# Performance work log

Hardware: AMD Instinct MI355X
Metric: run time of the kernel (lower is better)

The kernel has to match this reference:

```python
import jax, jax.numpy as jnp
import numpy as np

# dims: batch, length, n_values, input_dim, hidden_dim, embed_dim
B, L, V, D_IN, H, E = 8192, 32, 256, 256, 512, 256


def setup_inputs() -> dict:
    key = jax.random.key(0)
    ks = jax.random.split(key, 11)
    s = 0.05  # keep gates/tanh in a reasonable range
    return {
        "x": jax.random.normal(ks[0], (B, D_IN), jnp.float32),
        "emb": jax.random.normal(ks[1], (V, E), jnp.float32) * s,      # nn.Embedding weight
        "sos_embed": jax.random.normal(ks[2], (E,), jnp.float32) * s,
        "W_i2h": jax.random.normal(ks[3], (H, D_IN), jnp.float32) * s,  # input2hidden[0]
        "b_i2h": jax.random.normal(ks[4], (H,), jnp.float32) * s,
        "W_ih": jax.random.normal(ks[5], (3 * H, E), jnp.float32) * s,  # GRU weight_ih_l0 (r,z,n)
        "W_hh": jax.random.normal(ks[6], (3 * H, H), jnp.float32) * s,  # GRU weight_hh_l0
        "b_ih": jax.random.normal(ks[7], (3 * H,), jnp.float32) * s,
        "b_hh": jax.random.normal(ks[8], (3 * H,), jnp.float32) * s,
        "W_out": jax.random.normal(ks[9], (V, H), jnp.float32) * s,     # hidden2output
        "b_out": jax.random.normal(ks[10], (V,), jnp.float32) * s,
    }


def reference(x, emb, sos_embed, W_i2h, b_i2h, W_ih, W_hh, b_ih, b_hh, W_out, b_out):
    # Free-running decode (input=None), eval mode => argmax sampling.
    h0 = x @ W_i2h.T + b_i2h                                   # [B, H] initial hidden
    i0 = jnp.broadcast_to(sos_embed, (x.shape[0], sos_embed.shape[0]))  # [B, E]

    def step(carry, _):
        h, i = carry
        # PyTorch GRU cell: gates ordered (r, z, n)
        gi = i @ W_ih.T + b_ih                                  # [B, 3H]
        gh = h @ W_hh.T + b_hh                                  # [B, 3H]
        ir, iz, i_n = jnp.split(gi, 3, axis=-1)
        hr, hz, h_n = jnp.split(gh, 3, axis=-1)
        r = jax.nn.sigmoid(ir + hr)
        z = jax.nn.sigmoid(iz + hz)
        n = jnp.tanh(i_n + r * h_n)
        h_new = (1.0 - z) * n + z * h                           # [B, H]
        logit = h_new @ W_out.T + b_out                         # [B, V]
        tok = jnp.argmax(logit, axis=-1)                        # [B] int
        return (h_new, emb[tok]), (tok, logit)

    _, (toks, logits) = jax.lax.scan(step, (h0, i0), None, length=L)
    output = toks.T                                             # [B, L]
    logits = jnp.transpose(logits, (1, 0, 2))                   # [B, L, V]
    return output, logits
```

## Files before the change

kernel.cpp:

```cpp
#include <hip/hip_runtime.h>
#include <math.h>

namespace {

constexpr int kB  = 8192;
constexpr int kL  = 32;
constexpr int kV  = 256;
constexpr int kH  = 512;
constexpr int kE  = 256;
constexpr int kH3 = 1536;

__device__ __forceinline__ float sigm(float x) { return 1.0f / (1.0f + expf(-x)); }

__device__ __forceinline__ void gld_lds16(const float* g, float* lds) {
    __builtin_amdgcn_global_load_lds((const __attribute__((address_space(1))) void*)g,
                                     (__attribute__((address_space(3))) void*)lds, 16, 0, 0);
}
__device__ __forceinline__ void gld_lds4(const float* g, float* lds) {
    __builtin_amdgcn_global_load_lds((const __attribute__((address_space(1))) void*)g,
                                     (__attribute__((address_space(3))) void*)lds, 4, 0, 0);
}

__global__ __launch_bounds__(256) void transpose_kernel(
    const float* __restrict__ in, float* __restrict__ out, int R, int C)
{
    __shared__ float tile[32][33];
    const int tx = threadIdx.x & 31, ty = threadIdx.x >> 5;
    const int c0 = blockIdx.x * 32, r0 = blockIdx.y * 32;
#pragma unroll
    for (int i = 0; i < 4; ++i)
        tile[ty + i * 8][tx] = in[(size_t)(r0 + ty + i * 8) * C + c0 + tx];
    __syncthreads();
#pragma unroll
    for (int i = 0; i < 4; ++i)
        out[(size_t)(c0 + ty + i * 8) * R + r0 + tx] = tile[tx][ty + i * 8];
}

__global__ __launch_bounds__(256) void g_table_kernel(
    const float* __restrict__ emb, const float* __restrict__ sos,
    const float* __restrict__ W, const float* __restrict__ bias,
    float* __restrict__ G)
{
    __shared__ __align__(16) float As[32][64];
    __shared__ __align__(16) float Bs[32][64];
    const int tid = threadIdx.x;
    const int tn = tid & 15, tm = tid >> 4;
    const int m0 = blockIdx.x * 64;
    const int n0 = blockIdx.y * 64;
    float acc[4][4] = {};
    for (int kt = 0; kt < 8; ++kt) {
        const int k0 = kt * 32;
#pragma unroll
        for (int i = 0; i < 2; ++i) {
            int l = tid + i * 256;
            int r = l >> 3, kq = l & 7;
            int row = m0 + r;
            float4 v = make_float4(0.f, 0.f, 0.f, 0.f);
            if (row < 256)       v = *(const float4*)(emb + (size_t)row * kE + k0 + kq * 4);
            else if (row == 256) v = *(const float4*)(sos + k0 + kq * 4);
            As[kq*4+0][r] = v.x; As[kq*4+1][r] = v.y; As[kq*4+2][r] = v.z; As[kq*4+3][r] = v.w;
        }
#pragma unroll
        for (int i = 0; i < 2; ++i) {
            int l = tid + i * 256;
            int r = l >> 3, kq = l & 7;
            float4 v = *(const float4*)(W + (size_t)(n0 + r) * kE + k0 + kq * 4);
            Bs[kq*4+0][r] = v.x; Bs[kq*4+1][r] = v.y; Bs[kq*4+2][r] = v.z; Bs[kq*4+3][r] = v.w;
        }
        __syncthreads();
#pragma unroll
        for (int kk = 0; kk < 32; ++kk) {
            const float4 a = *(const float4*)(&As[kk][tm*4]);
            const float4 b = *(const float4*)(&Bs[kk][tn*4]);
            const float av[4] = {a.x, a.y, a.z, a.w};
            const float bv[4] = {b.x, b.y, b.z, b.w};
#pragma unroll
            for (int i = 0; i < 4; ++i)
#pragma unroll
                for (int j = 0; j < 4; ++j)
                    acc[i][j] = fmaf(av[i], bv[j], acc[i][j]);
        }
        __syncthreads();
    }
    const int cb = n0 + tn * 4;
    const float4 bb = *(const float4*)(bias + cb);
    const float bv[4] = {bb.x, bb.y, bb.z, bb.w};
#pragma unroll
    for (int i = 0; i < 4; ++i) {
        int row = m0 + tm * 4 + i;
        if (row < 257) {
            float4 o = make_float4(acc[i][0] + bv[0], acc[i][1] + bv[1],
                                   acc[i][2] + bv[2], acc[i][3] + bv[3]);
            *(float4*)(G + (size_t)row * kH3 + cb) = o;
        }
    }
}

__global__ __launch_bounds__(256) void h0_kernel(
    const float* __restrict__ x, const float* __restrict__ W,
    const float* __restrict__ bias, float* __restrict__ hT)
{
    __shared__ __align__(16) float As[32][64];
    __shared__ __align__(16) float Bs[32][64];
    const int tid = threadIdx.x;
    const int tn = tid & 15, tm = tid >> 4;
    const int m0 = blockIdx.x * 64;
    const int n0 = blockIdx.y * 64;
    float acc[4][4] = {};
    for (int kt = 0; kt < 8; ++kt) {
        const int k0 = kt * 32;
#pragma unroll
        for (int i = 0; i < 2; ++i) {
            int l = tid + i * 256;
            int r = l >> 3, kq = l & 7;
            float4 v = *(const float4*)(x + (size_t)(m0 + r) * kE + k0 + kq * 4);
            As[kq*4+0][r] = v.x; As[kq*4+1][r] = v.y; As[kq*4+2][r] = v.z; As[kq*4+3][r] = v.w;
        }
#pragma unroll
        for (int i = 0; i < 2; ++i) {
            int l = tid + i * 256;
            int r = l >> 3, kq = l & 7;
            float4 v = *(const float4*)(W + (size_t)(n0 + r) * kE + k0 + kq * 4);
            Bs[kq*4+0][r] = v.x; Bs[kq*4+1][r] = v.y; Bs[kq*4+2][r] = v.z; Bs[kq*4+3][r] = v.w;
        }
        __syncthreads();
#pragma unroll
        for (int kk = 0; kk < 32; ++kk) {
            const float4 a = *(const float4*)(&As[kk][tm*4]);
            const float4 b = *(const float4*)(&Bs[kk][tn*4]);
            const float av[4] = {a.x, a.y, a.z, a.w};
            const float bv[4] = {b.x, b.y, b.z, b.w};
#pragma unroll
            for (int i = 0; i < 4; ++i)
#pragma unroll
                for (int j = 0; j < 4; ++j)
                    acc[i][j] = fmaf(av[i], bv[j], acc[i][j]);
        }
        __syncthreads();
    }
    const int cb = n0 + tn * 4;
    const float4 bb = *(const float4*)(bias + cb);
    const float bv[4] = {bb.x, bb.y, bb.z, bb.w};
#pragma unroll
    for (int i = 0; i < 4; ++i) {
        int row = m0 + tm * 4 + i;
#pragma unroll
        for (int c = 0; c < 4; ++c)
            hT[(size_t)(cb + c) * kB + row] = acc[i][c] + bv[c];
    }
}

__global__ __launch_bounds__(256, 2) void gru_step_kernel(
    const float* __restrict__ hT_in, const float* __restrict__ W_hhT,
    const float* __restrict__ b_hh, const float* __restrict__ G,
    const int* __restrict__ tok, const int t, float* __restrict__ hT_out)
{
    __shared__ __align__(16) float As[2][32 * 128];
    __shared__ __align__(16) float Bs[2][32 * 96];
    const int tid = threadIdx.x;
    const int tn = tid & 15;
    const int tm = tid >> 4;
    const int b0 = blockIdx.x * 128;
    const int j0 = blockIdx.y * 32;

    float acc[8][3][2] = {};

    auto stage = [&](int kt, int buf) {
        const int k0 = kt * 32;
        float* as = As[buf];
        float* bs = Bs[buf];
#pragma unroll
        for (int i = 0; i < 4; ++i) {
            int l = tid + i * 256;
            int r = l >> 5, c = l & 31;
            gld_lds16(hT_in + (size_t)(k0 + r) * kB + b0 + c * 4, &as[4 * l]);
        }
#pragma unroll
        for (int i = 0; i < 3; ++i) {
            int l = tid + i * 256;
            int r = l / 24, q = l % 24;
            int g = q >> 3, cc = q & 7;
            gld_lds16(W_hhT + (size_t)(k0 + r) * kH3 + g * kH + j0 + cc * 4, &bs[4 * l]);
        }
    };

    stage(0, 0);
#pragma unroll 1
    for (int kt = 0; kt < 16; ++kt) {
        if (kt < 15) {
            stage(kt + 1, (kt + 1) & 1);
            asm volatile("s_waitcnt vmcnt(7)" ::: "memory");
        } else {
            asm volatile("s_waitcnt vmcnt(0)" ::: "memory");
        }
        __builtin_amdgcn_s_barrier();
        __builtin_amdgcn_sched_barrier(0);
        const float* __restrict__ as = As[kt & 1];
        const float* __restrict__ bs = Bs[kt & 1];
#pragma unroll 8
        for (int kk = 0; kk < 32; ++kk) {
            const float4 a0 = *(const float4*)&as[kk * 128 + tm * 8];
            const float4 a1 = *(const float4*)&as[kk * 128 + tm * 8 + 4];
            const float2 br = *(const float2*)&bs[kk * 96 + tn * 2];
            const float2 bz = *(const float2*)&bs[kk * 96 + 32 + tn * 2];
            const float2 bn = *(const float2*)&bs[kk * 96 + 64 + tn * 2];
            const float av[8] = {a0.x, a0.y, a0.z, a0.w, a1.x, a1.y, a1.z, a1.w};
#pragma unroll
            for (int i = 0; i < 8; ++i) {
                acc[i][0][0] = fmaf(av[i], br.x, acc[i][0][0]);
                acc[i][0][1] = fmaf(av[i], br.y, acc[i][0][1]);
                acc[i][1][0] = fmaf(av[i], bz.x, acc[i][1][0]);
                acc[i][1][1] = fmaf(av[i], bz.y, acc[i][1][1]);
                acc[i][2][0] = fmaf(av[i], bn.x, acc[i][2][0]);
                acc[i][2][1] = fmaf(av[i], bn.y, acc[i][2][1]);
            }
        }
        __builtin_amdgcn_sched_barrier(0);
        __builtin_amdgcn_s_barrier();
        __builtin_amdgcn_sched_barrier(0);
    }

    const int j  = j0 + tn * 2;
    const int bb = b0 + tm * 8;
    const float2 bhr = *(const float2*)&b_hh[j];
    const float2 bhz = *(const float2*)&b_hh[kH + j];
    const float2 bhn = *(const float2*)&b_hh[2 * kH + j];
    const float4 hp0a = *(const float4*)&hT_in[(size_t)j * kB + bb];
    const float4 hp0b = *(const float4*)&hT_in[(size_t)j * kB + bb + 4];
    const float4 hp1a = *(const float4*)&hT_in[(size_t)(j + 1) * kB + bb];
    const float4 hp1b = *(const float4*)&hT_in[(size_t)(j + 1) * kB + bb + 4];
    const float hp[2][8] = {
        {hp0a.x, hp0a.y, hp0a.z, hp0a.w, hp0b.x, hp0b.y, hp0b.z, hp0b.w},
        {hp1a.x, hp1a.y, hp1a.z, hp1a.w, hp1b.x, hp1b.y, hp1b.z, hp1b.w}};
    int rows[8];
    if (t == 0) {
#pragma unroll
        for (int i = 0; i < 8; ++i) rows[i] = 256;
    } else {
        const int4 t0 = *(const int4*)&tok[bb];
        const int4 t1 = *(const int4*)&tok[bb + 4];
        rows[0] = t0.x; rows[1] = t0.y; rows[2] = t0.z; rows[3] = t0.w;
        rows[4] = t1.x; rows[5] = t1.y; rows[6] = t1.z; rows[7] = t1.w;
    }
    float ho[2][8];
#pragma unroll
    for (int i = 0; i < 8; ++i) {
        const float* Gr = G + (size_t)rows[i] * kH3;
        const float2 gr = *(const float2*)&Gr[j];
        const float2 gz = *(const float2*)&Gr[kH + j];
        const float2 gn = *(const float2*)&Gr[2 * kH + j];
        float r0 = sigm(gr.x + acc[i][0][0] + bhr.x);
        float z0 = sigm(gz.x + acc[i][1][0] + bhz.x);
        float n0 = tanhf(gn.x + r0 * (acc[i][2][0] + bhn.x));
        ho[0][i] = (1.0f - z0) * n0 + z0 * hp[0][i];
        float r1 = sigm(gr.y + acc[i][0][1] + bhr.y);
        float z1 = sigm(gz.y + acc[i][1][1] + bhz.y);
        float n1 = tanhf(gn.y + r1 * (acc[i][2][1] + bhn.y));
        ho[1][i] = (1.0f - z1) * n1 + z1 * hp[1][i];
    }
    *(float4*)&hT_out[(size_t)j * kB + bb]           = make_float4(ho[0][0], ho[0][1], ho[0][2], ho[0][3]);
    *(float4*)&hT_out[(size_t)j * kB + bb + 4]       = make_float4(ho[0][4], ho[0][5], ho[0][6], ho[0][7]);
    *(float4*)&hT_out[(size_t)(j + 1) * kB + bb]     = make_float4(ho[1][0], ho[1][1], ho[1][2], ho[1][3]);
    *(float4*)&hT_out[(size_t)(j + 1) * kB + bb + 4] = make_float4(ho[1][4], ho[1][5], ho[1][6], ho[1][7]);
}

__global__ __launch_bounds__(512, 2) void logit_kernel(
    const float* __restrict__ hT, const float* __restrict__ W_outT,
    const float* __restrict__ b_out, int* __restrict__ tok,
    float* __restrict__ out_tok, float* __restrict__ out_logits, const int t)
{
    __shared__ __align__(16) float As[2][32 * 32];
    __shared__ __align__(16) float Bs[2][32 * 256];
    const int tid = threadIdx.x;
    const int tn = tid & 31;
    const int tm = tid >> 5;
    const int b0 = blockIdx.x * 32;
    float acc[2][8] = {};

    auto stage = [&](int kt, int buf) {
        const int k0 = kt * 32;
        float* as = As[buf];
        float* bs = Bs[buf];
#pragma unroll
        for (int i = 0; i < 4; ++i) {
            int l = tid + i * 512;
            int r = l >> 6, c = l & 63;
            gld_lds16(W_outT + (size_t)(k0 + r) * kV + c * 4, &bs[4 * l]);
        }
#pragma unroll
        for (int i = 0; i < 2; ++i) {
            int l = tid + i * 512;
            int r = l >> 5, c = l & 31;
            gld_lds4(hT + (size_t)(k0 + r) * kB + b0 + c, &as[l]);
        }
    };

    stage(0, 0);
#pragma unroll 1
    for (int kt = 0; kt < 16; ++kt) {
        if (kt < 15) {
            stage(kt + 1, (kt + 1) & 1);
            asm volatile("s_waitcnt vmcnt(6)" ::: "memory");
        } else {
            asm volatile("s_waitcnt vmcnt(0)" ::: "memory");
        }
        __builtin_amdgcn_s_barrier();
        __builtin_amdgcn_sched_barrier(0);
        const float* __restrict__ as = As[kt & 1];
        const float* __restrict__ bs = Bs[kt & 1];
#pragma unroll 8
        for (int kk = 0; kk < 32; ++kk) {
            const float2 a = *(const float2*)&as[kk * 32 + tm * 2];
#pragma unroll
            for (int m = 0; m < 8; ++m) {
                const float bv = bs[kk * 256 + tn + m * 32];
                acc[0][m] = fmaf(a.x, bv, acc[0][m]);
                acc[1][m] = fmaf(a.y, bv, acc[1][m]);
            }
        }
        __builtin_amdgcn_sched_barrier(0);
        __builtin_amdgcn_s_barrier();
        __builtin_amdgcn_sched_barrier(0);
    }

    float bo[8];
#pragma unroll
    for (int m = 0; m < 8; ++m) bo[m] = b_out[tn + m * 32];
#pragma unroll
    for (int i = 0; i < 2; ++i) {
        const int b = b0 + tm * 2 + i;
        float mx = -INFINITY; int mi = 0;
        float* lp = out_logits + ((size_t)b * kL + t) * kV;
#pragma unroll
        for (int m = 0; m < 8; ++m) {
            const int vi = tn + m * 32;
            const float v = acc[i][m] + bo[m];
            lp[vi] = v;
            if (v > mx) { mx = v; mi = vi; }
        }
#pragma unroll
        for (int s = 16; s >= 1; s >>= 1) {
            float pm = __shfl_xor(mx, s, 64);
            int   pi = __shfl_xor(mi, s, 64);
            if (pm > mx || (pm == mx && pi < mi)) { mx = pm; mi = pi; }
        }
        if (tn == 0) {
            tok[b] = mi;
            out_tok[(size_t)b * kL + t] = (float)mi;
        }
    }
}

}

extern "C" void kernel_launch(void* const* d_in, const int* in_sizes, int n_in,
                              void* d_out, int out_size, void* d_ws, size_t ws_size,
                              hipStream_t stream) {
    const float* x      = (const float*)d_in[0];
    const float* emb    = (const float*)d_in[1];
    const float* sos    = (const float*)d_in[2];
    const float* W_i2h  = (const float*)d_in[3];
    const float* b_i2h  = (const float*)d_in[4];
    const float* W_ih   = (const float*)d_in[5];
    const float* W_hh   = (const float*)d_in[6];
    const float* b_ih   = (const float*)d_in[7];
    const float* b_hh   = (const float*)d_in[8];
    const float* W_out  = (const float*)d_in[9];
    const float* b_out  = (const float*)d_in[10];

    float* out        = (float*)d_out;
    float* out_tok    = out;
    float* out_logits = out + (size_t)kB * kL;

    float* hA     = (float*)d_ws;
    float* hB     = hA + (size_t)kH * kB;
    float* G      = hB + (size_t)kH * kB;
    float* W_hhT  = G + (size_t)257 * kH3;
    float* W_outT = W_hhT + (size_t)kH * kH3;
    int*   tok    = (int*)(W_outT + (size_t)kH * kV);

    transpose_kernel<<<dim3(kH / 32, kH3 / 32), 256, 0, stream>>>(W_hh, W_hhT, kH3, kH);
    transpose_kernel<<<dim3(kH / 32, kV / 32), 256, 0, stream>>>(W_out, W_outT, kV, kH);
    g_table_kernel<<<dim3(5, kH3 / 64), 256, 0, stream>>>(emb, sos, W_ih, b_ih, G);
    h0_kernel<<<dim3(kB / 64, kH / 64), 256, 0, stream>>>(x, W_i2h, b_i2h, hA);

    for (int t = 0; t < kL; ++t) {
        float* hin  = (t & 1) ? hB : hA;
        float* hout = (t & 1) ? hA : hB;
        gru_step_kernel<<<dim3(kB / 128, kH / 32), 256, 0, stream>>>(
            hin, W_hhT, b_hh, G, tok, t, hout);
        logit_kernel<<<dim3(kB / 32), 512, 0, stream>>>(
            hout, W_outT, b_out, tok, out_tok, out_logits, t);
    }
}
```

Before: 7.290 ms.

## Widen GRU step tile to 64 hidden columns per block with K=16 stages

The GRU recurrent GEMM tile grows from 128x32 to 128x64 hidden units per block, so each thread holds 8x3x4 accumulators instead of 8x3x2. The K stage depth is halved to 16 to keep LDS usage unchanged, with the pipelined wait count adjusted to match. The aim is more FMAs per LDS read and half as many blocks re-reading the h tile. The cost is higher register pressure (96 accumulators) at launch_bounds(256,2), twice as many barrier-separated K stages, and half as many blocks in the grid (512 instead of 1024).

```diff
diff --git a/kernel.cpp b/kernel.cpp
--- a/kernel.cpp
+++ b/kernel.cpp
@@ -155,22 +155,22 @@
     const float* __restrict__ b_hh, const float* __restrict__ G,
     const int* __restrict__ tok, const int t, float* __restrict__ hT_out)
 {
-    __shared__ __align__(16) float As[2][32 * 128];
-    __shared__ __align__(16) float Bs[2][32 * 96];
+    __shared__ __align__(16) float As[2][16 * 128];
+    __shared__ __align__(16) float Bs[2][16 * 192];
     const int tid = threadIdx.x;
     const int tn = tid & 15;
     const int tm = tid >> 4;
     const int b0 = blockIdx.x * 128;
-    const int j0 = blockIdx.y * 32;
-
-    float acc[8][3][2] = {};
+    const int j0 = blockIdx.y * 64;
+
+    float acc[8][3][4] = {};
 
     auto stage = [&](int kt, int buf) {
-        const int k0 = kt * 32;
+        const int k0 = kt * 16;
         float* as = As[buf];
         float* bs = Bs[buf];
 #pragma unroll
-        for (int i = 0; i < 4; ++i) {
+        for (int i = 0; i < 2; ++i) {
             int l = tid + i * 256;
             int r = l >> 5, c = l & 31;
             gld_lds16(hT_in + (size_t)(k0 + r) * kB + b0 + c * 4, &as[4 * l]);
@@ -178,18 +178,18 @@
 #pragma unroll
         for (int i = 0; i < 3; ++i) {
             int l = tid + i * 256;
-            int r = l / 24, q = l % 24;
-            int g = q >> 3, cc = q & 7;
+            int r = l / 48, q = l % 48;
+            int g = q >> 4, cc = q & 15;
             gld_lds16(W_hhT + (size_t)(k0 + r) * kH3 + g * kH + j0 + cc * 4, &bs[4 * l]);
         }
     };
 
     stage(0, 0);
 #pragma unroll 1
-    for (int kt = 0; kt < 16; ++kt) {
-        if (kt < 15) {
+    for (int kt = 0; kt < 32; ++kt) {
+        if (kt < 31) {
             stage(kt + 1, (kt + 1) & 1);
-            asm volatile("s_waitcnt vmcnt(7)" ::: "memory");
+            asm volatile("s_waitcnt vmcnt(5)" ::: "memory");
         } else {
             asm volatile("s_waitcnt vmcnt(0)" ::: "memory");
         }
@@ -197,41 +197,49 @@
         __builtin_amdgcn_sched_barrier(0);
         const float* __restrict__ as = As[kt & 1];
         const float* __restrict__ bs = Bs[kt & 1];
-#pragma unroll 8
-        for (int kk = 0; kk < 32; ++kk) {
+#pragma unroll
+        for (int kk = 0; kk < 16; ++kk) {
             const float4 a0 = *(const float4*)&as[kk * 128 + tm * 8];
             const float4 a1 = *(const float4*)&as[kk * 128 + tm * 8 + 4];
-            const float2 br = *(const float2*)&bs[kk * 96 + tn * 2];
-            const float2 bz = *(const float2*)&bs[kk * 96 + 32 + tn * 2];
-            const float2 bn = *(const float2*)&bs[kk * 96 + 64 + tn * 2];
-            const float av[8] = {a0.x, a0.y, a0.z, a0.w, a1.x, a1.y, a1.z, a1.w};
-#pragma unroll
-            for (int i = 0; i < 8; ++i) {
-                acc[i][0][0] = fmaf(av[i], br.x, acc[i][0][0]);
-                acc[i][0][1] = fmaf(av[i], br.y, acc[i][0][1]);
-                acc[i][1][0] = fmaf(av[i], bz.x, acc[i][1][0]);
-                acc[i][1][1] = fmaf(av[i], bz.y, acc[i][1][1]);
-                acc[i][2][0] = fmaf(av[i], bn.x, acc[i][2][0]);
-                acc[i][2][1] = fmaf(av[i], bn.y, acc[i][2][1]);
-            }
+            const float4 br = *(const float4*)&bs[kk * 192 + tn * 4];
+            const float4 bz = *(const float4*)&bs[kk * 192 + 64 + tn * 4];
+            const float4 bn = *(const float4*)&bs[kk * 192 + 128 + tn * 4];
+            const float av[8]  = {a0.x, a0.y, a0.z, a0.w, a1.x, a1.y, a1.z, a1.w};
+            const float brv[4] = {br.x, br.y, br.z, br.w};
+            const float bzv[4] = {bz.x, bz.y, bz.z, bz.w};
+            const float bnv[4] = {bn.x, bn.y, bn.z, bn.w};
+#pragma unroll
+            for (int i = 0; i < 8; ++i)
+#pragma unroll
+                for (int jj = 0; jj < 4; ++jj) {
+                    acc[i][0][jj] = fmaf(av[i], brv[jj], acc[i][0][jj]);
+                    acc[i][1][jj] = fmaf(av[i], bzv[jj], acc[i][1][jj]);
+                    acc[i][2][jj] = fmaf(av[i], bnv[jj], acc[i][2][jj]);
+                }
         }
         __builtin_amdgcn_sched_barrier(0);
         __builtin_amdgcn_s_barrier();
         __builtin_amdgcn_sched_barrier(0);
     }
 
-    const int j  = j0 + tn * 2;
+    const int j  = j0 + tn * 4;
     const int bb = b0 + tm * 8;
-    const float2 bhr = *(const float2*)&b_hh[j];
-    const float2 bhz = *(const float2*)&b_hh[kH + j];
-    const float2 bhn = *(const float2*)&b_hh[2 * kH + j];
-    const float4 hp0a = *(const float4*)&hT_in[(size_t)j * kB + bb];
-    const float4 hp0b = *(const float4*)&hT_in[(size_t)j * kB + bb + 4];
-    const float4 hp1a = *(const float4*)&hT_in[(size_t)(j + 1) * kB + bb];
-    const float4 hp1b = *(const float4*)&hT_in[(size_t)(j + 1) * kB + bb + 4];
-    const float hp[2][8] = {
-        {hp0a.x, hp0a.y, hp0a.z, hp0a.w, hp0b.x, hp0b.y, hp0b.z, hp0b.w},
-        {hp1a.x, hp1a.y, hp1a.z, hp1a.w, hp1b.x, hp1b.y, hp1b.z, hp1b.w}};
+    const float4 bhr = *(const float4*)&b_hh[j];
+    const float4 bhz = *(const float4*)&b_hh[kH + j];
+    const float4 bhn = *(const float4*)&b_hh[2 * kH + j];
+    const float bhrv[4] = {bhr.x, bhr.y, bhr.z, bhr.w};
+    const float bhzv[4] = {bhz.x, bhz.y, bhz.z, bhz.w};
+    const float bhnv[4] = {bhn.x, bhn.y, bhn.z, bhn.w};
+
+    float hp[4][8];
+#pragma unroll
+    for (int jj = 0; jj < 4; ++jj) {
+        const float4 p0 = *(const float4*)&hT_in[(size_t)(j + jj) * kB + bb];
+        const float4 p1 = *(const float4*)&hT_in[(size_t)(j + jj) * kB + bb + 4];
+        hp[jj][0] = p0.x; hp[jj][1] = p0.y; hp[jj][2] = p0.z; hp[jj][3] = p0.w;
+        hp[jj][4] = p1.x; hp[jj][5] = p1.y; hp[jj][6] = p1.z; hp[jj][7] = p1.w;
+    }
+
     int rows[8];
     if (t == 0) {
 #pragma unroll
@@ -242,26 +250,32 @@
         rows[0] = t0.x; rows[1] = t0.y; rows[2] = t0.z; rows[3] = t0.w;
         rows[4] = t1.x; rows[5] = t1.y; rows[6] = t1.z; rows[7] = t1.w;
     }
-    float ho[2][8];
+
+    float ho[4][8];
 #pragma unroll
     for (int i = 0; i < 8; ++i) {
         const float* Gr = G + (size_t)rows[i] * kH3;
-        const float2 gr = *(const float2*)&Gr[j];
-        const float2 gz = *(const float2*)&Gr[kH + j];
-        const float2 gn = *(const float2*)&Gr[2 * kH + j];
-        float r0 = sigm(gr.x + acc[i][0][0] + bhr.x);
-        float z0 = sigm(gz.x + acc[i][1][0] + bhz.x);
-        float n0 = tanhf(gn.x + r0 * (acc[i][2][0] + bhn.x));
-        ho[0][i] = (1.0f - z0) * n0 + z0 * hp[0][i];
-        float r1 = sigm(gr.y + acc[i][0][1] + bhr.y);
-        float z1 = sigm(gz.y + acc[i][1][1] + bhz.y);
-        float n1 = tanhf(gn.y + r1 * (acc[i][2][1] + bhn.y));
-        ho[1][i] = (1.0f - z1) * n1 + z1 * hp[1][i];
-    }
-    *(float4*)&hT_out[(size_t)j * kB + bb]           = make_float4(ho[0][0], ho[0][1], ho[0][2], ho[0][3]);
-    *(float4*)&hT_out[(size_t)j * kB + bb + 4]       = make_float4(ho[0][4], ho[0][5], ho[0][6], ho[0][7]);
-    *(float4*)&hT_out[(size_t)(j + 1) * kB + bb]     = make_float4(ho[1][0], ho[1][1], ho[1][2], ho[1][3]);
-    *(float4*)&hT_out[(size_t)(j + 1) * kB + bb + 4] = make_float4(ho[1][4], ho[1][5], ho[1][6], ho[1][7]);
+        const float4 gr = *(const float4*)&Gr[j];
+        const float4 gz = *(const float4*)&Gr[kH + j];
+        const float4 gn = *(const float4*)&Gr[2 * kH + j];
+        const float grv[4] = {gr.x, gr.y, gr.z, gr.w};
+        const float gzv[4] = {gz.x, gz.y, gz.z, gz.w};
+        const float gnv[4] = {gn.x, gn.y, gn.z, gn.w};
+#pragma unroll
+        for (int jj = 0; jj < 4; ++jj) {
+            float r = sigm(grv[jj] + acc[i][0][jj] + bhrv[jj]);
+            float z = sigm(gzv[jj] + acc[i][1][jj] + bhzv[jj]);
+            float n = tanhf(gnv[jj] + r * (acc[i][2][jj] + bhnv[jj]));
+            ho[jj][i] = (1.0f - z) * n + z * hp[jj][i];
+        }
+    }
+#pragma unroll
+    for (int jj = 0; jj < 4; ++jj) {
+        *(float4*)&hT_out[(size_t)(j + jj) * kB + bb]     =
+            make_float4(ho[jj][0], ho[jj][1], ho[jj][2], ho[jj][3]);
+        *(float4*)&hT_out[(size_t)(j + jj) * kB + bb + 4] =
+            make_float4(ho[jj][4], ho[jj][5], ho[jj][6], ho[jj][7]);
+    }
 }
 
 __global__ __launch_bounds__(512, 2) void logit_kernel(
@@ -387,7 +401,7 @@
     for (int t = 0; t < kL; ++t) {
         float* hin  = (t & 1) ? hB : hA;
         float* hout = (t & 1) ? hA : hB;
-        gru_step_kernel<<<dim3(kB / 128, kH / 32), 256, 0, stream>>>(
+        gru_step_kernel<<<dim3(kB / 128, kH / 64), 256, 0, stream>>>(
             hin, W_hhT, b_hh, G, tok, t, hout);
         logit_kernel<<<dim3(kB / 32), 512, 0, stream>>>(
             hout, W_outT, b_out, tok, out_tok, out_logits, t);
```

After: 6.994 ms. 4.1% less time.
